# Performance work log

Measured on AMD Instinct MI355X. Metric: run time of the kernel, lower is better.

## Reference

```python
import jax, jax.numpy as jnp
import numpy as np

B, S, H = 2, 2048, 4096
NH, NKV, HD = 32, 8, 128
N_REP = NH // NKV
ROPE_BASE = 10000.0
NEG_INF = -1e9


def setup_inputs() -> dict:
    key = jax.random.key(0)
    k1, k2, k3, k4, k5 = jax.random.split(key, 5)
    hidden_states = jax.random.normal(k1, (B, S, H), dtype=jnp.float32)
    # standard prefill positions 0..S-1 for each batch row
    position_ids = jnp.tile(jnp.arange(S, dtype=jnp.int64)[None, :], (B, 1))
    # additive causal mask, broadcastable over batch and heads
    causal = jnp.tril(jnp.ones((S, S), dtype=bool))
    attention_mask = jnp.where(causal, 0.0, NEG_INF).astype(jnp.float32)[None, None]
    scale = 0.02
    Wq = jax.random.normal(k2, (H, NH * HD), dtype=jnp.float32) * scale
    Wk = jax.random.normal(k3, (H, NKV * HD), dtype=jnp.float32) * scale
    Wv = jax.random.normal(k4, (H, NKV * HD), dtype=jnp.float32) * scale
    Wo = jax.random.normal(k5, (NH * HD, H), dtype=jnp.float32) * scale
    return {"hidden_states": hidden_states, "position_ids": position_ids,
            "attention_mask": attention_mask, "Wq": Wq, "Wk": Wk, "Wv": Wv, "Wo": Wo}


def _rope_cos_sin(position_ids):
    # inv_freq: [HD/2]
    inv_freq = 1.0 / (ROPE_BASE ** (jnp.arange(0, HD, 2, dtype=jnp.float32) / HD))
    freqs = position_ids.astype(jnp.float32)[:, :, None] * inv_freq[None, None, :]  # [B,S,HD/2]
    emb = jnp.concatenate([freqs, freqs], axis=-1)  # [B,S,HD]
    # unsqueeze head dim (unsqueeze_dim=1)
    return jnp.cos(emb)[:, None], jnp.sin(emb)[:, None]  # [B,1,S,HD]


def _rotate_half(x):
    x1, x2 = jnp.split(x, 2, axis=-1)
    return jnp.concatenate([-x2, x1], axis=-1)


def reference(hidden_states, position_ids, attention_mask, Wq, Wk, Wv, Wo):
    b, s, _ = hidden_states.shape
    q = jnp.einsum('bsh,hd->bsd', hidden_states, Wq).reshape(b, s, NH, HD).transpose(0, 2, 1, 3)
    k = jnp.einsum('bsh,hd->bsd', hidden_states, Wk).reshape(b, s, NKV, HD).transpose(0, 2, 1, 3)
    v = jnp.einsum('bsh,hd->bsd', hidden_states, Wv).reshape(b, s, NKV, HD).transpose(0, 2, 1, 3)

    cos, sin = _rope_cos_sin(position_ids)  # [B,1,S,HD]
    q = q * cos + _rotate_half(q) * sin
    k = k * cos + _rotate_half(k) * sin

    # GQA: repeat each kv head N_REP times consecutively -> [B,NH,S,HD]
    k = jnp.repeat(k, N_REP, axis=1)
    v = jnp.repeat(v, N_REP, axis=1)

    scores = jnp.einsum('bhqd,bhkd->bhqk', q, k) / np.sqrt(HD).astype(np.float32)
    scores = scores + attention_mask
    attn = jax.nn.softmax(scores, axis=-1)
    out = jnp.einsum('bhqk,bhkd->bhqd', attn, v)  # [B,NH,S,HD]
    out = out.transpose(0, 2, 1, 3).reshape(b, s, NH * HD)
    return out @ Wo
```

## Files before the change

kernel.cpp:

```cpp
#include <hip/hip_runtime.h>
#include <hip/hip_bf16.h>
#include <stdint.h>
#include <math.h>

#define S_LEN 2048
#define NHEAD 32
#define NKVH  8
#define HDIM  128
#define HID   4096

typedef __attribute__((ext_vector_type(4))) float f32x4;
typedef __attribute__((ext_vector_type(8))) short s16x8;
typedef __attribute__((ext_vector_type(4))) short s16x4;

__device__ __forceinline__ float bf2f(ushort u){
  union { float f; uint32_t i; } c; c.i = ((uint32_t)u) << 16; return c.f;
}
__device__ __forceinline__ ushort f2bf(float f){
  union { float f; uint32_t i; } c; c.f = f;
  uint32_t i = c.i;
  return (ushort)((i + 0x7FFFu + ((i >> 16) & 1u)) >> 16);
}

__device__ __forceinline__ void wtrans_body(const float* __restrict__ W, ushort* __restrict__ WT,
                                            int K, int N, int k0, int n0, int tid){
  __shared__ float T[64][68];
  #pragma unroll
  for (int it = 0; it < 4; ++it){
    int slot = it*256 + tid;
    int kr = slot >> 4, c4 = slot & 15;
    f32x4 v = *(const f32x4*)(W + (size_t)(k0 + kr) * N + n0 + c4*4);
    *(f32x4*)&T[kr][c4*4] = v;
  }
  __syncthreads();
  #pragma unroll
  for (int it = 0; it < 2; ++it){
    int slot = it*256 + tid;
    int nr = slot >> 3, k8 = slot & 7;
    s16x8 o;
    #pragma unroll
    for (int j = 0; j < 8; ++j) o[j] = f2bf(T[k8*8 + j][nr]);
    *(s16x8*)(WT + (size_t)(n0 + nr) * K + k0 + k8*8) = o;
  }
}

__global__ void prep_k(const float* __restrict__ Wq, const float* __restrict__ Wk,
                       const float* __restrict__ Wv, const float* __restrict__ Wo,
                       ushort* __restrict__ WqT, ushort* __restrict__ WkvT,
                       ushort* __restrict__ WoT,
                       const float* __restrict__ X, ushort* __restrict__ Xb,
                       float* __restrict__ cost, float* __restrict__ sint){
  int y = blockIdx.y;
  if (y < 160){
    const float* W; ushort* WT; int N, n0;
    if (y < 64){ W = Wq; WT = WqT;  N = 4096; n0 = y*64; }
    else if (y < 80){ W = Wk; WT = WkvT; N = 1024; n0 = (y-64)*64; }
    else if (y < 96){ W = Wv; WT = WkvT + (size_t)1024*HID; N = 1024; n0 = (y-80)*64; }
    else { W = Wo; WT = WoT; N = 4096; n0 = (y-96)*64; }
    wtrans_body(W, WT, HID, N, blockIdx.x*64, n0, threadIdx.x);
  } else {
    int cid = (y - 160) * 64 + blockIdx.x;
    int ri = cid * 256 + threadIdx.x;
    if (ri < S_LEN * 64){
      int s = ri >> 6, j = ri & 63;
      float invf = powf(10000.0f, -(float)j * (1.0f / 64.0f));
      float a = (float)s * invf;
      cost[ri] = cosf(a);
      sint[ri] = sinf(a);
    }
    size_t i = ((size_t)cid * 256 + threadIdx.x) * 8;
    f32x4 a = *(const f32x4*)(X + i);
    f32x4 b = *(const f32x4*)(X + i + 4);
    s16x8 o;
    o[0]=f2bf(a[0]); o[1]=f2bf(a[1]); o[2]=f2bf(a[2]); o[3]=f2bf(a[3]);
    o[4]=f2bf(b[0]); o[5]=f2bf(b[1]); o[6]=f2bf(b[2]); o[7]=f2bf(b[3]);
    *(s16x8*)(Xb + i) = o;
  }
}

template<int EPI>
__global__ __launch_bounds__(256)
void gemm_bt(const ushort* __restrict__ A, const ushort* __restrict__ Bt,
             void* __restrict__ Cout, int M, int N, int K,
             const float* __restrict__ cost, const float* __restrict__ sint,
             float oscale, ushort* __restrict__ Vt)
{
  __shared__ ushort As[2][128*64];
  __shared__ ushort Bs[2][128*64];
  const int tid = threadIdx.x;
  const int w = tid >> 6, lane = tid & 63;
  const int l15 = lane & 15, l4 = lane >> 4;
  const int swz = (l15 & 7) << 4;
  const size_t Abase = (size_t)blockIdx.x * 128 * K;
  const size_t Bbase = (size_t)blockIdx.y * 128 * K;

  f32x4 acc[2][8] = {};

  const int srow = (w << 3) + (lane >> 3);
  const int scolb = ((lane & 7) * 16) ^ (((lane >> 3) & 7) << 4);
  const ushort* Agrow = A + Abase + (size_t)srow * K;
  const ushort* Bgrow = Bt + Bbase + (size_t)srow * K;

  auto STAGE = [&](int bf, int k0){
    #pragma unroll
    for (int i = 0; i < 4; ++i){
      __builtin_amdgcn_global_load_lds(
        (const __attribute__((address_space(1))) void*)((const char*)(Agrow + k0 + (size_t)(32*i)*K) + scolb),
        (__attribute__((address_space(3))) void*)((char*)As[bf] + w*1024 + i*4096), 16, 0, 0);
      __builtin_amdgcn_global_load_lds(
        (const __attribute__((address_space(1))) void*)((const char*)(Bgrow + k0 + (size_t)(32*i)*K) + scolb),
        (__attribute__((address_space(3))) void*)((char*)Bs[bf] + w*1024 + i*4096), 16, 0, 0);
    }
  };

  const int nt = K >> 6;
  int cur = 0;
  STAGE(0, 0);
  __syncthreads();

  for (int t = 0; t < nt; ++t){
    if (t + 1 < nt) STAGE(cur ^ 1, (t + 1) * 64);
    #pragma unroll
    for (int kk = 0; kk < 2; ++kk){
      s16x8 af[2], bfr[8];
      #pragma unroll
      for (int m = 0; m < 2; ++m)
        af[m] = *(const s16x8*)((char*)As[cur] + (w*32 + m*16 + l15)*128 + ((kk*64 + l4*16) ^ swz));
      #pragma unroll
      for (int n = 0; n < 8; ++n)
        bfr[n] = *(const s16x8*)((char*)Bs[cur] + (n*16 + l15)*128 + ((kk*64 + l4*16) ^ swz));
      __builtin_amdgcn_s_setprio(1);
      #pragma unroll
      for (int m = 0; m < 2; ++m)
        #pragma unroll
        for (int n = 0; n < 8; ++n)
          acc[m][n] = __builtin_amdgcn_mfma_f32_16x16x32_bf16(af[m], bfr[n], acc[m][n], 0, 0, 0);
      __builtin_amdgcn_s_setprio(0);
    }
    __syncthreads();
    cur ^= 1;
  }

  const int r0 = (int)blockIdx.x * 128 + w * 32;
  const int c0 = (int)blockIdx.y * 128;
  if (EPI == 2){
    float* C = (float*)Cout;
    #pragma unroll
    for (int m = 0; m < 2; ++m)
      #pragma unroll
      for (int r = 0; r < 4; ++r){
        size_t rowoff = (size_t)(r0 + m*16 + l4*4 + r) * N + c0;
        #pragma unroll
        for (int n = 0; n < 8; ++n)
          C[rowoff + n*16 + l15] = acc[m][n][r];
      }
  } else if (EPI == 0){
    ushort* C = (ushort*)Cout;
    #pragma unroll
    for (int m = 0; m < 2; ++m)
      #pragma unroll
      for (int r = 0; r < 4; ++r){
        size_t rowoff = (size_t)(r0 + m*16 + l4*4 + r) * N + c0;
        #pragma unroll
        for (int n = 0; n < 8; ++n)
          C[rowoff + n*16 + l15] = f2bf(acc[m][n][r]);
      }
  } else if (EPI == 3 && c0 >= 1024){
    const int kvh = (c0 - 1024) >> 7;
    #pragma unroll
    for (int m = 0; m < 2; ++m){
      int row0 = r0 + m*16 + l4*4;
      int b = row0 >> 11, s = row0 & (S_LEN - 1);
      ushort* vbase = Vt + ((size_t)(b*NKVH + kvh) * HDIM) * S_LEN + s;
      #pragma unroll
      for (int n = 0; n < 8; ++n){
        s16x4 pk;
        #pragma unroll
        for (int r = 0; r < 4; ++r) pk[r] = (short)f2bf(acc[m][n][r]);
        *(s16x4*)(vbase + (size_t)(n*16 + l15) * S_LEN) = pk;
      }
    }
  } else {
    ushort* C = (ushort*)Cout;
    #pragma unroll
    for (int m = 0; m < 2; ++m)
      #pragma unroll
      for (int r = 0; r < 4; ++r){
        int row = r0 + m*16 + l4*4 + r;
        int pos = row & (S_LEN - 1);
        size_t rowoff = (size_t)row * N + c0;
        #pragma unroll
        for (int n = 0; n < 4; ++n){
          int d = n*16 + l15;
          float cv = cost[pos*64 + d];
          float sv = sint[pos*64 + d];
          float x1 = acc[m][n][r];
          float x2 = acc[m][n+4][r];
          C[rowoff + d]      = f2bf((x1*cv - x2*sv) * oscale);
          C[rowoff + d + 64] = f2bf((x2*cv + x1*sv) * oscale);
        }
      }
  }
}

template<int EPI>
__global__ __launch_bounds__(512, 2)
void gemm256(const ushort* __restrict__ A, const ushort* __restrict__ Bt,
             void* __restrict__ Cout, int M, int N, int K,
             const float* __restrict__ cost, const float* __restrict__ sint,
             float oscale)
{
  extern __shared__ char L[];
  const int tid = threadIdx.x;
  const int wid = tid >> 6, lane = tid & 63;
  const int wm = wid >> 2, wn = wid & 3;
  const int l15 = lane & 15, l4 = lane >> 4;
  const int swz = (l15 & 7) << 4;
  const int nwg  = gridDim.x;
  const int bid  = blockIdx.x;
  const int sbid = (bid & 7) * (nwg >> 3) + (bid >> 3);
  const int gx   = sbid & 15, gy = sbid >> 4;
  const int brow = gx * 256, bcol = gy * 256;
  const int nt = K >> 6;

  f32x4 acc[8][4] = {};
  s16x8 areg[8], b0reg[4], b1reg[4];

  auto STAGE = [&](int arr, int sh, int bf, int tile){
    int tt = tile < nt ? tile : nt - 1;
    const ushort* gb = arr ? (Bt + (size_t)bcol * K) : (A + (size_t)brow * K);
    char* lb = L + bf*65536 + arr*32768;
    #pragma unroll
    for (int j = 0; j < 2; ++j){
      int c   = j*8 + wid;
      int rg0 = (c >= 8 ? 128 : 0) + sh*64 + ((c*8) & 63);
      int rg  = rg0 + (lane >> 3);
      const char* gsrc = (const char*)(gb + (size_t)rg * K + tt*64)
                       + (((lane & 7) * 16) ^ (((lane >> 3) & 7) << 4));
      __builtin_amdgcn_global_load_lds(
        (const __attribute__((address_space(1))) void*)gsrc,
        (__attribute__((address_space(3))) void*)(lb + rg0*128), 16, 0, 0);
    }
  };
  auto LDA = [&](int bf, int mh){
    const char* ab = L + bf*65536;
    #pragma unroll
    for (int i = 0; i < 4; ++i){
      int row = wm*128 + (mh*4 + i)*16 + l15;
      #pragma unroll
      for (int kk = 0; kk < 2; ++kk)
        areg[i*2+kk] = *(const s16x8*)(ab + row*128 + ((kk*64 + l4*16) ^ swz));
    }
  };
  auto LDB = [&](int bf, int nh, s16x8* breg){
    const char* bb = L + bf*65536 + 32768;
    #pragma unroll
    for (int j = 0; j < 2; ++j){
      int row = wn*64 + (nh*2 + j)*16 + l15;
      #pragma unroll
      for (int kk = 0; kk < 2; ++kk)
        breg[j*2+kk] = *(const s16x8*)(bb + row*128 + ((kk*64 + l4*16) ^ swz));
    }
  };
  auto MFMA16 = [&](int mh, int nh, s16x8* breg){
    __builtin_amdgcn_s_setprio(1);
    #pragma unroll
    for (int kk = 0; kk < 2; ++kk)
      #pragma unroll
      for (int i = 0; i < 4; ++i)
        #pragma unroll
        for (int j = 0; j < 2; ++j)
          acc[mh*4+i][nh*2+j] = __builtin_amdgcn_mfma_f32_16x16x32_bf16(
              areg[i*2+kk], breg[j*2+kk], acc[mh*4+i][nh*2+j], 0, 0, 0);
    __builtin_amdgcn_s_setprio(0);
  };

  STAGE(0,0,0,0); STAGE(1,0,0,0); STAGE(0,1,0,0); STAGE(1,1,0,0);
  STAGE(0,0,1,1); STAGE(1,0,1,1); STAGE(0,1,1,1);
  asm volatile("s_waitcnt vmcnt(6)" ::: "memory");
  __builtin_amdgcn_s_barrier();

  for (int t = 0; t < nt; t += 2){
    LDA(0,0); LDB(0,0,b0reg); STAGE(1,1,1,t+1);
    __builtin_amdgcn_s_barrier();
    MFMA16(0,0,b0reg);
    LDB(0,1,b1reg); STAGE(0,0,0,t+2);
    __builtin_amdgcn_s_barrier();
    MFMA16(0,1,b1reg);
    LDA(0,1); STAGE(1,0,0,t+2);
    __builtin_amdgcn_s_barrier();
    MFMA16(1,0,b0reg);
    STAGE(0,1,0,t+2);
    asm volatile("s_waitcnt vmcnt(6)" ::: "memory");
    __builtin_amdgcn_s_barrier();
    MFMA16(1,1,b1reg);
    LDA(1,0); LDB(1,0,b0reg); STAGE(1,1,0,t+2);
    __builtin_amdgcn_s_barrier();
    MFMA16(0,0,b0reg);
    LDB(1,1,b1reg); STAGE(0,0,1,t+3);
    __builtin_amdgcn_s_barrier();
    MFMA16(0,1,b1reg);
    LDA(1,1); STAGE(1,0,1,t+3);
    __builtin_amdgcn_s_barrier();
    MFMA16(1,0,b0reg);
    STAGE(0,1,1,t+3);
    asm volatile("s_waitcnt vmcnt(6)" ::: "memory");
    __builtin_amdgcn_s_barrier();
    MFMA16(1,1,b1reg);
  }
  asm volatile("s_waitcnt vmcnt(0)" ::: "memory");
  __builtin_amdgcn_s_barrier();

  if (EPI == 2){
    float* C = (float*)Cout;
    #pragma unroll
    for (int m = 0; m < 8; ++m)
      #pragma unroll
      for (int r = 0; r < 4; ++r){
        size_t rowoff = (size_t)(brow + wm*128 + m*16 + l4*4 + r) * N + bcol + wn*64;
        #pragma unroll
        for (int n = 0; n < 4; ++n)
          C[rowoff + n*16 + l15] = acc[m][n][r];
      }
  } else {
    float* xls = (float*)L;
    ushort* C = (ushort*)Cout;
    float* mine = xls + wid*2176;
    const float* part = xls + (wid^1)*2176;
    #pragma unroll
    for (int mm = 0; mm < 4; ++mm){
      #pragma unroll
      for (int mi = 0; mi < 2; ++mi){
        int m = mm*2 + mi;
        #pragma unroll
        for (int r = 0; r < 4; ++r)
          #pragma unroll
          for (int n = 0; n < 4; ++n)
            mine[(mi*16 + l4*4 + r)*68 + n*16 + l15] = acc[m][n][r];
      }
      __builtin_amdgcn_s_barrier();
      #pragma unroll
      for (int mi = 0; mi < 2; ++mi){
        int m = mm*2 + mi;
        #pragma unroll
        for (int r = 0; r < 4; ++r){
          int rr = brow + wm*128 + m*16 + l4*4 + r;
          int pos = rr & (S_LEN - 1);
          size_t rowoff = (size_t)rr * N + bcol + wn*64;
          #pragma unroll
          for (int n = 0; n < 4; ++n){
            int d2 = n*16 + l15;
            float x  = acc[m][n][r];
            float px = part[(mi*16 + l4*4 + r)*68 + d2];
            float cv = cost[pos*64 + d2], sv = sint[pos*64 + d2];
            float o = (wn & 1) ? (x*cv + px*sv) : (x*cv - px*sv);
            C[rowoff + d2] = f2bf(o * oscale);
          }
        }
      }
      __builtin_amdgcn_s_barrier();
    }
  }
}

__global__ __launch_bounds__(256, 2)
void attn_k(const ushort* __restrict__ Q, const ushort* __restrict__ KVb,
            const ushort* __restrict__ Vt, ushort* __restrict__ AO)
{
  extern __shared__ char L[];
  const int tid = threadIdx.x, w = tid >> 6, lane = tid & 63;
  const int l15 = lane & 15, l4 = lane >> 4;
  const int swz = (l15 & 7) << 4;

  const int id  = blockIdx.x;
  const int idx = id >> 3;
  const int bk  = (id & 7) * 2 + (idx & 1);
  const int b   = bk >> 3, kvh = bk & 7;
  const int h   = kvh * 4 + ((idx >> 1) & 3);
  const int pair= idx >> 3;

  const char* Kgb = (const char*)(KVb + (size_t)b * S_LEN * 2048 + kvh * HDIM);
  const char* Vgb = (const char*)(Vt + (size_t)bk * HDIM * S_LEN);
  char* pb = L + 65536 + w*4096;

  const int krow_in = lane >> 4;
  const int kbyte   = l15 * 16;
  const int vrow_in = lane >> 3;
  const int vbyte   = (lane & 7) * 16;

  auto STAGE = [&](int kv0, int bf){
    char* kb = L + bf*32768;
    char* vb = kb + 16384;
    #pragma unroll
    for (int i = 0; i < 4; ++i){
      int c = w*4 + i;
      int krow = c*4 + krow_in;
      const char* ksrc = Kgb + (size_t)(kv0 + krow) * 4096 + (kbyte ^ ((krow & 7) << 4));
      __builtin_amdgcn_global_load_lds(
        (const __attribute__((address_space(1))) void*)ksrc,
        (__attribute__((address_space(3))) void*)(kb + c*1024), 16, 0, 0);
      int vrow = c*8 + vrow_in;
      const char* vsrc = Vgb + (size_t)vrow * (S_LEN*2) + kv0*2 + (vbyte ^ ((vrow & 7) << 4));
      __builtin_amdgcn_global_load_lds(
        (const __attribute__((address_space(1))) void*)vsrc,
        (__attribute__((address_space(3))) void*)(vb + c*1024), 16, 0, 0);
    }
  };

  #pragma unroll
  for (int half = 0; half < 2; ++half){
    const int qt  = half ? (15 - pair) : pair;
    const int wq0 = qt * 128 + w * 32;
    const int nt  = 2*qt + 2;

    s16x8 qf[2][4];
    #pragma unroll
    for (int m = 0; m < 2; ++m){
      const ushort* qp = Q + (size_t)(b*S_LEN + wq0 + m*16 + l15) * (NHEAD*HDIM) + h*HDIM + l4*8;
      #pragma unroll
      for (int kk = 0; kk < 4; ++kk)
        qf[m][kk] = *(const s16x8*)(qp + kk*32);
    }

    float mreg0 = -1e30f, mreg1 = -1e30f, lreg0 = 0.f, lreg1 = 0.f;
    f32x4 oacc[2][8] = {};
    const int qlane0 = wq0 + l15, qlane1 = qlane0 + 16;

    int cur = 0;
    STAGE(0, 0);
    __syncthreads();

    for (int t = 0; t < nt; ++t){
      const int kv0 = t * 64;
      if (t + 1 < nt) STAGE(kv0 + 64, cur ^ 1);
      if (kv0 <= wq0 + 31){
        const char* kb = L + cur*32768;
        const char* vb = kb + 16384;
        f32x4 st[4][2] = {};
        #pragma unroll
        for (int kk = 0; kk < 4; ++kk){
          s16x8 kf[4];
          #pragma unroll
          for (int i = 0; i < 4; ++i){
            int row = i*16 + l15;
            kf[i] = *(const s16x8*)(kb + row*256 + ((kk*64 + l4*16) ^ swz));
          }
          __builtin_amdgcn_s_setprio(1);
          #pragma unroll
          for (int i = 0; i < 4; ++i){
            st[i][0] = __builtin_amdgcn_mfma_f32_16x16x32_bf16(kf[i], qf[0][kk], st[i][0], 0, 0, 0);
            st[i][1] = __builtin_amdgcn_mfma_f32_16x16x32_bf16(kf[i], qf[1][kk], st[i][1], 0, 0, 0);
          }
          __builtin_amdgcn_s_setprio(0);
        }
        if (kv0 + 63 > wq0){
          #pragma unroll
          for (int i = 0; i < 4; ++i){
            int kvb = kv0 + i*16 + l4*4;
            #pragma unroll
            for (int r = 0; r < 4; ++r){
              if (kvb + r > qlane0) st[i][0][r] = -1e30f;
              if (kvb + r > qlane1) st[i][1][r] = -1e30f;
            }
          }
        }
        float mx0 = -1e30f, mx1 = -1e30f;
        #pragma unroll
        for (int i = 0; i < 4; ++i){
          mx0 = fmaxf(mx0, fmaxf(fmaxf(st[i][0][0], st[i][0][1]), fmaxf(st[i][0][2], st[i][0][3])));
          mx1 = fmaxf(mx1, fmaxf(fmaxf(st[i][1][0], st[i][1][1]), fmaxf(st[i][1][2], st[i][1][3])));
        }
        mx0 = fmaxf(mx0, __shfl_xor(mx0, 16)); mx0 = fmaxf(mx0, __shfl_xor(mx0, 32));
        mx1 = fmaxf(mx1, __shfl_xor(mx1, 16)); mx1 = fmaxf(mx1, __shfl_xor(mx1, 32));
        bool resc = !__all((mx0 <= mreg0 + 8.0f) & (mx1 <= mreg1 + 8.0f));
        if (resc){
          float mn0 = fmaxf(mreg0, mx0), mn1 = fmaxf(mreg1, mx1);
          float fs0 = __expf(mreg0 - mn0), fs1 = __expf(mreg1 - mn1);
          mreg0 = mn0; mreg1 = mn1; lreg0 *= fs0; lreg1 *= fs1;
          #pragma unroll
          for (int m = 0; m < 2; ++m){
            float fsm = m ? fs1 : fs0;
            #pragma unroll
            for (int r = 0; r < 4; ++r){
              float fb = __shfl(fsm, (lane & 48) | (l4*4 + r));
              #pragma unroll
              for (int n = 0; n < 8; ++n) oacc[m][n][r] *= fb;
            }
          }
        }
        float s0 = 0.f, s1 = 0.f;
        #pragma unroll
        for (int i = 0; i < 4; ++i){
          int col2 = (i*16 + l4*4) * 2;
          f32x4 p0, p1;
          #pragma unroll
          for (int r = 0; r < 4; ++r){
            p0[r] = __expf(st[i][0][r] - mreg0); s0 += p0[r];
            p1[r] = __expf(st[i][1][r] - mreg1); s1 += p1[r];
          }
          s16x4 u0, u1;
          #pragma unroll
          for (int r = 0; r < 4; ++r){ u0[r] = (short)f2bf(p0[r]); u1[r] = (short)f2bf(p1[r]); }
          *(s16x4*)(pb + ((l15*128 + col2) ^ swz))        = u0;
          *(s16x4*)(pb + (((16 + l15)*128 + col2) ^ swz)) = u1;
        }
        lreg0 += s0; lreg1 += s1;
        #pragma unroll
        for (int kk = 0; kk < 2; ++kk){
          s16x8 pf0 = *(const s16x8*)(pb + ((l15*128 + kk*64 + l4*16) ^ swz));
          s16x8 pf1 = *(const s16x8*)(pb + (((16 + l15)*128 + kk*64 + l4*16) ^ swz));
          s16x8 vf[8];
          #pragma unroll
          for (int n = 0; n < 8; ++n){
            int row = n*16 + l15;
            vf[n] = *(const s16x8*)(vb + row*128 + ((kk*64 + l4*16) ^ swz));
          }
          __builtin_amdgcn_s_setprio(1);
          #pragma unroll
          for (int n = 0; n < 8; ++n){
            oacc[0][n] = __builtin_amdgcn_mfma_f32_16x16x32_bf16(pf0, vf[n], oacc[0][n], 0, 0, 0);
            oacc[1][n] = __builtin_amdgcn_mfma_f32_16x16x32_bf16(pf1, vf[n], oacc[1][n], 0, 0, 0);
          }
          __builtin_amdgcn_s_setprio(0);
        }
      }
      __syncthreads();
      cur ^= 1;
    }

    lreg0 += __shfl_xor(lreg0, 16); lreg0 += __shfl_xor(lreg0, 32);
    lreg1 += __shfl_xor(lreg1, 16); lreg1 += __shfl_xor(lreg1, 32);
    float inv0 = 1.0f / lreg0, inv1 = 1.0f / lreg1;
    #pragma unroll
    for (int m = 0; m < 2; ++m){
      float invm = m ? inv1 : inv0;
      #pragma unroll
      for (int r = 0; r < 4; ++r){
        float ib = __shfl(invm, (lane & 48) | (l4*4 + r));
        ushort* dst = AO + (size_t)(b*S_LEN + wq0 + m*16 + l4*4 + r) * (NHEAD*HDIM) + h*HDIM;
        #pragma unroll
        for (int n = 0; n < 8; ++n)
          dst[n*16 + l15] = f2bf(oacc[m][n][r] * ib);
      }
    }
  }
}

extern "C" void kernel_launch(void* const* d_in, const int* in_sizes, int n_in,
                              void* d_out, int out_size, void* d_ws, size_t ws_size,
                              hipStream_t stream)
{
  const float* X  = (const float*)d_in[0];
  const float* Wq = (const float*)d_in[3];
  const float* Wk = (const float*)d_in[4];
  const float* Wv = (const float*)d_in[5];
  const float* Wo = (const float*)d_in[6];

  char* ws = (char*)d_ws;
  float*  cost = (float*) (ws + 0);
  float*  sint = (float*) (ws + 524288);
  ushort* Xb   = (ushort*)(ws + 1048576);
  ushort* WqT  = (ushort*)(ws + 34603008);
  ushort* WkvT = (ushort*)(ws + 68157440);
  ushort* Qb   = (ushort*)(ws + 84934656);
  ushort* KVb  = (ushort*)(ws + 118489088);
  ushort* Vt   = (ushort*)(ws + 135266304);
  ushort* WoT  = (ushort*)(ws + 143654912);
  ushort* AO   = WqT;

  const float qk_scale = 0.08838834764831845f;

  const int GLDS = 131072;
  const int ALDS = 81920;
  hipFuncSetAttribute((const void*)gemm256<1>, hipFuncAttributeMaxDynamicSharedMemorySize, GLDS);
  hipFuncSetAttribute((const void*)gemm256<2>, hipFuncAttributeMaxDynamicSharedMemorySize, GLDS);
  hipFuncSetAttribute((const void*)attn_k,     hipFuncAttributeMaxDynamicSharedMemorySize, ALDS);

  prep_k<<<dim3(64, 288), 256, 0, stream>>>(Wq, Wk, Wv, Wo, WqT, WkvT, WoT, X, Xb, cost, sint);

  gemm256<1><<<256, 512, GLDS, stream>>>(Xb, WqT, Qb, 4096, 4096, 4096, cost, sint, qk_scale);
  gemm_bt<3><<<dim3(32, 16), 256, 0, stream>>>(Xb, WkvT, KVb, 4096, 2048, 4096, cost, sint, 1.0f, Vt);

  attn_k<<<512, 256, ALDS, stream>>>(Qb, KVb, Vt, AO);

  gemm256<2><<<256, 512, GLDS, stream>>>(AO, WoT, d_out, 4096, 4096, 4096, nullptr, nullptr, 1.0f);
}
```

Before: 469.1 us.

## Process both paired causal query tiles in one KV sweep sharing staged K/V

Instead of running two sequential passes over KV (one for the short query tile, one for the long one), the kernel keeps both query tiles' state live and feeds each staged K/V block to both tiles in a single loop. This removes the redundant reloading of the first KV blocks and one pipeline restart, and the short tile's work overlaps with the long tile's. In exchange it doubles the accumulator and Q-fragment register footprint (two 2x8 f32x4 output sets), which under launch_bounds(256,2) risks spills or lower occupancy.

New measurement: 628.2 us. +33.9%, slower.

```diff
diff --git a/kernel.cpp b/kernel.cpp
--- a/kernel.cpp
+++ b/kernel.cpp
@@ -378,6 +378,10 @@
   const int b   = bk >> 3, kvh = bk & 7;
   const int h   = kvh * 4 + ((idx >> 1) & 3);
   const int pair= idx >> 3;
+  const int qtA = pair, qtB = 15 - pair;
+  const int wqA = qtA * 128 + w * 32;
+  const int wqB = qtB * 128 + w * 32;
+  const int nt  = 2*qtB + 2;
 
   const char* Kgb = (const char*)(KVb + (size_t)b * S_LEN * 2048 + kvh * HDIM);
   const char* Vgb = (const char*)(Vt + (size_t)bk * HDIM * S_LEN);
@@ -407,130 +411,136 @@
     }
   };
 
+  s16x8 qfA[2][4], qfB[2][4];
   #pragma unroll
-  for (int half = 0; half < 2; ++half){
-    const int qt  = half ? (15 - pair) : pair;
-    const int wq0 = qt * 128 + w * 32;
-    const int nt  = 2*qt + 2;
-
-    s16x8 qf[2][4];
-    #pragma unroll
-    for (int m = 0; m < 2; ++m){
-      const ushort* qp = Q + (size_t)(b*S_LEN + wq0 + m*16 + l15) * (NHEAD*HDIM) + h*HDIM + l4*8;
-      #pragma unroll
-      for (int kk = 0; kk < 4; ++kk)
-        qf[m][kk] = *(const s16x8*)(qp + kk*32);
-    }
-
-    float mreg0 = -1e30f, mreg1 = -1e30f, lreg0 = 0.f, lreg1 = 0.f;
-    f32x4 oacc[2][8] = {};
+  for (int m = 0; m < 2; ++m){
+    const ushort* qpA = Q + (size_t)(b*S_LEN + wqA + m*16 + l15) * (NHEAD*HDIM) + h*HDIM + l4*8;
+    const ushort* qpB = Q + (size_t)(b*S_LEN + wqB + m*16 + l15) * (NHEAD*HDIM) + h*HDIM + l4*8;
+    #pragma unroll
+    for (int kk = 0; kk < 4; ++kk){
+      qfA[m][kk] = *(const s16x8*)(qpA + kk*32);
+      qfB[m][kk] = *(const s16x8*)(qpB + kk*32);
+    }
+  }
+
+  float mA0 = -1e30f, mA1 = -1e30f, lA0 = 0.f, lA1 = 0.f;
+  float mB0 = -1e30f, mB1 = -1e30f, lB0 = 0.f, lB1 = 0.f;
+  f32x4 oA[2][8] = {}, oB[2][8] = {};
+
+  auto TILE = [&](int kv0, const char* kb, const char* vb, s16x8 (&qf)[2][4],
+                  float& m0, float& m1, float& l0, float& l1,
+                  f32x4 (&oacc)[2][8], int wq0){
     const int qlane0 = wq0 + l15, qlane1 = qlane0 + 16;
-
-    int cur = 0;
-    STAGE(0, 0);
+    f32x4 st[4][2] = {};
+    #pragma unroll
+    for (int kk = 0; kk < 4; ++kk){
+      s16x8 kf[4];
+      #pragma unroll
+      for (int i = 0; i < 4; ++i){
+        int row = i*16 + l15;
+        kf[i] = *(const s16x8*)(kb + row*256 + ((kk*64 + l4*16) ^ swz));
+      }
+      __builtin_amdgcn_s_setprio(1);
+      #pragma unroll
+      for (int i = 0; i < 4; ++i){
+        st[i][0] = __builtin_amdgcn_mfma_f32_16x16x32_bf16(kf[i], qf[0][kk], st[i][0], 0, 0, 0);
+        st[i][1] = __builtin_amdgcn_mfma_f32_16x16x32_bf16(kf[i], qf[1][kk], st[i][1], 0, 0, 0);
+      }
+      __builtin_amdgcn_s_setprio(0);
+    }
+    if (kv0 + 63 > wq0){
+      #pragma unroll
+      for (int i = 0; i < 4; ++i){
+        int kvb = kv0 + i*16 + l4*4;
+        #pragma unroll
+        for (int r = 0; r < 4; ++r){
+          if (kvb + r > qlane0) st[i][0][r] = -1e30f;
+          if (kvb + r > qlane1) st[i][1][r] = -1e30f;
+        }
+      }
+    }
+    float mx0 = -1e30f, mx1 = -1e30f;
+    #pragma unroll
+    for (int i = 0; i < 4; ++i){
+      mx0 = fmaxf(mx0, fmaxf(fmaxf(st[i][0][0], st[i][0][1]), fmaxf(st[i][0][2], st[i][0][3])));
+      mx1 = fmaxf(mx1, fmaxf(fmaxf(st[i][1][0], st[i][1][1]), fmaxf(st[i][1][2], st[i][1][3])));
+    }
+    mx0 = fmaxf(mx0, __shfl_xor(mx0, 16)); mx0 = fmaxf(mx0, __shfl_xor(mx0, 32));
+    mx1 = fmaxf(mx1, __shfl_xor(mx1, 16)); mx1 = fmaxf(mx1, __shfl_xor(mx1, 32));
+    bool resc = !__all((mx0 <= m0 + 8.0f) & (mx1 <= m1 + 8.0f));
+    if (resc){
+      float mn0 = fmaxf(m0, mx0), mn1 = fmaxf(m1, mx1);
+      float fs0 = __expf(m0 - mn0), fs1 = __expf(m1 - mn1);
+      m0 = mn0; m1 = mn1; l0 *= fs0; l1 *= fs1;
+      #pragma unroll
+      for (int m = 0; m < 2; ++m){
+        float fsm = m ? fs1 : fs0;
+        #pragma unroll
+        for (int r = 0; r < 4; ++r){
+          float fb = __shfl(fsm, (lane & 48) | (l4*4 + r));
+          #pragma unroll
+          for (int n = 0; n < 8; ++n) oacc[m][n][r] *= fb;
+        }
+      }
+    }
+    float s0 = 0.f, s1 = 0.f;
+    #pragma unroll
+    for (int i = 0; i < 4; ++i){
+      int col2 = (i*16 + l4*4) * 2;
+      f32x4 p0, p1;
+      #pragma unroll
+      for (int r = 0; r < 4; ++r){
+        p0[r] = __expf(st[i][0][r] - m0); s0 += p0[r];
+        p1[r] = __expf(st[i][1][r] - m1); s1 += p1[r];
+      }
+      s16x4 u0, u1;
+      #pragma unroll
+      for (int r = 0; r < 4; ++r){ u0[r] = (short)f2bf(p0[r]); u1[r] = (short)f2bf(p1[r]); }
+      *(s16x4*)(pb + ((l15*128 + col2) ^ swz))        = u0;
+      *(s16x4*)(pb + (((16 + l15)*128 + col2) ^ swz)) = u1;
+    }
+    l0 += s0; l1 += s1;
+    #pragma unroll
+    for (int kk = 0; kk < 2; ++kk){
+      s16x8 pf0 = *(const s16x8*)(pb + ((l15*128 + kk*64 + l4*16) ^ swz));
+      s16x8 pf1 = *(const s16x8*)(pb + (((16 + l15)*128 + kk*64 + l4*16) ^ swz));
+      s16x8 vf[8];
+      #pragma unroll
+      for (int n = 0; n < 8; ++n){
+        int row = n*16 + l15;
+        vf[n] = *(const s16x8*)(vb + row*128 + ((kk*64 + l4*16) ^ swz));
+      }
+      __builtin_amdgcn_s_setprio(1);
+      #pragma unroll
+      for (int n = 0; n < 8; ++n){
+        oacc[0][n] = __builtin_amdgcn_mfma_f32_16x16x32_bf16(pf0, vf[n], oacc[0][n], 0, 0, 0);
+        oacc[1][n] = __builtin_amdgcn_mfma_f32_16x16x32_bf16(pf1, vf[n], oacc[1][n], 0, 0, 0);
+      }
+      __builtin_amdgcn_s_setprio(0);
+    }
+  };
+
+  int cur = 0;
+  STAGE(0, 0);
+  __syncthreads();
+
+  for (int t = 0; t < nt; ++t){
+    const int kv0 = t * 64;
+    if (t + 1 < nt) STAGE(kv0 + 64, cur ^ 1);
+    const char* kb = L + cur*32768;
+    const char* vb = kb + 16384;
+    if (kv0 <= wqA + 31)
+      TILE(kv0, kb, vb, qfA, mA0, mA1, lA0, lA1, oA, wqA);
+    if (kv0 <= wqB + 31)
+      TILE(kv0, kb, vb, qfB, mB0, mB1, lB0, lB1, oB, wqB);
     __syncthreads();
-
-    for (int t = 0; t < nt; ++t){
-      const int kv0 = t * 64;
-      if (t + 1 < nt) STAGE(kv0 + 64, cur ^ 1);
-      if (kv0 <= wq0 + 31){
-        const char* kb = L + cur*32768;
-        const char* vb = kb + 16384;
-        f32x4 st[4][2] = {};
-        #pragma unroll
-        for (int kk = 0; kk < 4; ++kk){
-          s16x8 kf[4];
-          #pragma unroll
-          for (int i = 0; i < 4; ++i){
-            int row = i*16 + l15;
-            kf[i] = *(const s16x8*)(kb + row*256 + ((kk*64 + l4*16) ^ swz));
-          }
-          __builtin_amdgcn_s_setprio(1);
-          #pragma unroll
-          for (int i = 0; i < 4; ++i){
-            st[i][0] = __builtin_amdgcn_mfma_f32_16x16x32_bf16(kf[i], qf[0][kk], st[i][0], 0, 0, 0);
-            st[i][1] = __builtin_amdgcn_mfma_f32_16x16x32_bf16(kf[i], qf[1][kk], st[i][1], 0, 0, 0);
-          }
-          __builtin_amdgcn_s_setprio(0);
-        }
-        if (kv0 + 63 > wq0){
-          #pragma unroll
-          for (int i = 0; i < 4; ++i){
-            int kvb = kv0 + i*16 + l4*4;
-            #pragma unroll
-            for (int r = 0; r < 4; ++r){
-              if (kvb + r > qlane0) st[i][0][r] = -1e30f;
-              if (kvb + r > qlane1) st[i][1][r] = -1e30f;
-            }
-          }
-        }
-        float mx0 = -1e30f, mx1 = -1e30f;
-        #pragma unroll
-        for (int i = 0; i < 4; ++i){
-          mx0 = fmaxf(mx0, fmaxf(fmaxf(st[i][0][0], st[i][0][1]), fmaxf(st[i][0][2], st[i][0][3])));
-          mx1 = fmaxf(mx1, fmaxf(fmaxf(st[i][1][0], st[i][1][1]), fmaxf(st[i][1][2], st[i][1][3])));
-        }
-        mx0 = fmaxf(mx0, __shfl_xor(mx0, 16)); mx0 = fmaxf(mx0, __shfl_xor(mx0, 32));
-        mx1 = fmaxf(mx1, __shfl_xor(mx1, 16)); mx1 = fmaxf(mx1, __shfl_xor(mx1, 32));
-        bool resc = !__all((mx0 <= mreg0 + 8.0f) & (mx1 <= mreg1 + 8.0f));
-        if (resc){
-          float mn0 = fmaxf(mreg0, mx0), mn1 = fmaxf(mreg1, mx1);
-          float fs0 = __expf(mreg0 - mn0), fs1 = __expf(mreg1 - mn1);
-          mreg0 = mn0; mreg1 = mn1; lreg0 *= fs0; lreg1 *= fs1;
-          #pragma unroll
-          for (int m = 0; m < 2; ++m){
-            float fsm = m ? fs1 : fs0;
-            #pragma unroll
-            for (int r = 0; r < 4; ++r){
-              float fb = __shfl(fsm, (lane & 48) | (l4*4 + r));
-              #pragma unroll
-              for (int n = 0; n < 8; ++n) oacc[m][n][r] *= fb;
-            }
-          }
-        }
-        float s0 = 0.f, s1 = 0.f;
-        #pragma unroll
-        for (int i = 0; i < 4; ++i){
-          int col2 = (i*16 + l4*4) * 2;
-          f32x4 p0, p1;
-          #pragma unroll
-          for (int r = 0; r < 4; ++r){
-            p0[r] = __expf(st[i][0][r] - mreg0); s0 += p0[r];
-            p1[r] = __expf(st[i][1][r] - mreg1); s1 += p1[r];
-          }
-          s16x4 u0, u1;
-          #pragma unroll
-          for (int r = 0; r < 4; ++r){ u0[r] = (short)f2bf(p0[r]); u1[r] = (short)f2bf(p1[r]); }
-          *(s16x4*)(pb + ((l15*128 + col2) ^ swz))        = u0;
-          *(s16x4*)(pb + (((16 + l15)*128 + col2) ^ swz)) = u1;
-        }
-        lreg0 += s0; lreg1 += s1;
-        #pragma unroll
-        for (int kk = 0; kk < 2; ++kk){
-          s16x8 pf0 = *(const s16x8*)(pb + ((l15*128 + kk*64 + l4*16) ^ swz));
-          s16x8 pf1 = *(const s16x8*)(pb + (((16 + l15)*128 + kk*64 + l4*16) ^ swz));
-          s16x8 vf[8];
-          #pragma unroll
-          for (int n = 0; n < 8; ++n){
-            int row = n*16 + l15;
-            vf[n] = *(const s16x8*)(vb + row*128 + ((kk*64 + l4*16) ^ swz));
-          }
-          __builtin_amdgcn_s_setprio(1);
-          #pragma unroll
-          for (int n = 0; n < 8; ++n){
-            oacc[0][n] = __builtin_amdgcn_mfma_f32_16x16x32_bf16(pf0, vf[n], oacc[0][n], 0, 0, 0);
-            oacc[1][n] = __builtin_amdgcn_mfma_f32_16x16x32_bf16(pf1, vf[n], oacc[1][n], 0, 0, 0);
-          }
-          __builtin_amdgcn_s_setprio(0);
-        }
-      }
-      __syncthreads();
-      cur ^= 1;
-    }
-
-    lreg0 += __shfl_xor(lreg0, 16); lreg0 += __shfl_xor(lreg0, 32);
-    lreg1 += __shfl_xor(lreg1, 16); lreg1 += __shfl_xor(lreg1, 32);
-    float inv0 = 1.0f / lreg0, inv1 = 1.0f / lreg1;
+    cur ^= 1;
+  }
+
+  auto EPI = [&](float l0, float l1, f32x4 (&oacc)[2][8], int wq0){
+    l0 += __shfl_xor(l0, 16); l0 += __shfl_xor(l0, 32);
+    l1 += __shfl_xor(l1, 16); l1 += __shfl_xor(l1, 32);
+    float inv0 = 1.0f / l0, inv1 = 1.0f / l1;
     #pragma unroll
     for (int m = 0; m < 2; ++m){
       float invm = m ? inv1 : inv0;
@@ -543,7 +553,9 @@
           dst[n*16 + l15] = f2bf(oacc[m][n][r] * ib);
       }
     }
-  }
+  };
+  EPI(lA0, lA1, oA, wqA);
+  EPI(lB0, lB1, oB, wqB);
 }
 
 extern "C" void kernel_launch(void* const* d_in, const int* in_sizes, int n_in,
```

## Remap GEMM wave column tiles so RoPE pairs stay in registers

Applied to the files above, without the earlier changes.

Changes which B-tile columns each wave owns so that every wave holds both halves (d and d+64) of a head's RoPE pair in its own accumulators. The RoPE epilogue can then be applied directly from registers, which removes the LDS round-trip exchange between partner waves and its barriers. The fp32 output path is updated to the same column mapping. Stores are now split across two 32-column chunks per wave, which may slightly change write coalescing.

New measurement: 464.0 us. About the same (-1.1%).

```diff
diff --git a/kernel.cpp b/kernel.cpp
--- a/kernel.cpp
+++ b/kernel.cpp
@@ -222,6 +222,7 @@
   const int gx   = sbid & 15, gy = sbid >> 4;
   const int brow = gx * 256, bcol = gy * 256;
   const int nt = K >> 6;
+  const int nbase = (wn >> 1)*128 + (wn & 1)*32;
 
   f32x4 acc[8][4] = {};
   s16x8 areg[8], b0reg[4], b1reg[4];
@@ -256,7 +257,8 @@
     const char* bb = L + bf*65536 + 32768;
     #pragma unroll
     for (int j = 0; j < 2; ++j){
-      int row = wn*64 + (nh*2 + j)*16 + l15;
+      int nb  = nh*2 + j;
+      int row = nbase + (nb & 1)*16 + (nb >> 1)*64 + l15;
       #pragma unroll
       for (int kk = 0; kk < 2; ++kk)
         breg[j*2+kk] = *(const s16x8*)(bb + row*128 + ((kk*64 + l4*16) ^ swz));
@@ -317,49 +319,32 @@
     for (int m = 0; m < 8; ++m)
       #pragma unroll
       for (int r = 0; r < 4; ++r){
-        size_t rowoff = (size_t)(brow + wm*128 + m*16 + l4*4 + r) * N + bcol + wn*64;
+        size_t rowoff = (size_t)(brow + wm*128 + m*16 + l4*4 + r) * N + bcol + nbase + l15;
         #pragma unroll
         for (int n = 0; n < 4; ++n)
-          C[rowoff + n*16 + l15] = acc[m][n][r];
+          C[rowoff + (n & 1)*16 + (n >> 1)*64] = acc[m][n][r];
       }
   } else {
-    float* xls = (float*)L;
     ushort* C = (ushort*)Cout;
-    float* mine = xls + wid*2176;
-    const float* part = xls + (wid^1)*2176;
-    #pragma unroll
-    for (int mm = 0; mm < 4; ++mm){
-      #pragma unroll
-      for (int mi = 0; mi < 2; ++mi){
-        int m = mm*2 + mi;
-        #pragma unroll
-        for (int r = 0; r < 4; ++r)
-          #pragma unroll
-          for (int n = 0; n < 4; ++n)
-            mine[(mi*16 + l4*4 + r)*68 + n*16 + l15] = acc[m][n][r];
-      }
-      __builtin_amdgcn_s_barrier();
-      #pragma unroll
-      for (int mi = 0; mi < 2; ++mi){
-        int m = mm*2 + mi;
-        #pragma unroll
-        for (int r = 0; r < 4; ++r){
-          int rr = brow + wm*128 + m*16 + l4*4 + r;
-          int pos = rr & (S_LEN - 1);
-          size_t rowoff = (size_t)rr * N + bcol + wn*64;
-          #pragma unroll
-          for (int n = 0; n < 4; ++n){
-            int d2 = n*16 + l15;
-            float x  = acc[m][n][r];
-            float px = part[(mi*16 + l4*4 + r)*68 + d2];
-            float cv = cost[pos*64 + d2], sv = sint[pos*64 + d2];
-            float o = (wn & 1) ? (x*cv + px*sv) : (x*cv - px*sv);
-            C[rowoff + d2] = f2bf(o * oscale);
-          }
-        }
-      }
-      __builtin_amdgcn_s_barrier();
-    }
+    const int hb = bcol + (wn >> 1)*128;
+    #pragma unroll
+    for (int m = 0; m < 8; ++m)
+      #pragma unroll
+      for (int r = 0; r < 4; ++r){
+        int rr = brow + wm*128 + m*16 + l4*4 + r;
+        int pos = rr & (S_LEN - 1);
+        size_t rowoff = (size_t)rr * N + hb;
+        #pragma unroll
+        for (int n = 0; n < 2; ++n){
+          int d2 = (wn & 1)*32 + n*16 + l15;
+          float cv = cost[pos*64 + d2];
+          float sv = sint[pos*64 + d2];
+          float x1 = acc[m][n][r];
+          float x2 = acc[m][n+2][r];
+          C[rowoff + d2]      = f2bf((x1*cv - x2*sv) * oscale);
+          C[rowoff + d2 + 64] = f2bf((x2*cv + x1*sv) * oscale);
+        }
+      }
   }
 }
 
```
